# Optimization experiments

Measured on AMD Instinct MI355X. Metric: run time of the kernel, lower is better.

The kernel has to match this reference:

```python
import jax, jax.numpy as jnp
import numpy as np

K = 5
P = 1.5
MU = 0.01
N_NODES = 100000
N_EDGES = 1600000
D_FEAT = 32


def setup_inputs() -> dict:
    key = jax.random.key(0)
    k1, k2 = jax.random.split(key)
    h = jax.random.normal(k1, (N_NODES, D_FEAT), dtype=jnp.float32)
    edge_index = jax.random.randint(k2, (2, N_EDGES), 0, N_NODES, dtype=jnp.int64)
    return {"h": h, "edge_index": edge_index}


def reference(h, edge_index):
    row, col = edge_index[0], edge_index[1]
    for _ in range(K):
        diff = h[row] - h[col]                      # [E, d] gather
        norm_diff = jnp.maximum(jnp.linalg.norm(diff, axis=1), 1e-6)  # [E]
        weights = (norm_diff / norm_diff.max()) ** (P - 2.0)          # [E]
        # agg[r] += sum over edges with row==r of weights * (h[col] - h[row])
        msgs = weights[:, None] * (-diff)           # [E, d]
        agg = jax.ops.segment_sum(msgs, row, num_segments=N_NODES)    # [N, d]
        h = h - MU * agg
    return h
```

## Files before the change

kernel.cpp:

```cpp
#include <hip/hip_runtime.h>

#define NN 100000
#define NE 1600000
#define DF 32
#define KIT 5
#define MU 0.01f
#define NSLOT 256
#define NV4 (NN * DF / 4)
#define ELLW 36
#define AUXCAP 65536
#define NSLICE 8
#define SLICEN (NN / NSLICE)
#define NBLKA (NE / 256)
#define SEGW 64

typedef float f32x4 __attribute__((ext_vector_type(4)));


__global__ __launch_bounds__(256) void zero_kernel(int* __restrict__ p, int n) {
    int i = blockIdx.x * blockDim.x + threadIdx.x;
    if (i < n) p[i] = 0;
}

__global__ __launch_bounds__(256) void ell_part_kernel(const int* __restrict__ row,
                                                       const int* __restrict__ col,
                                                       unsigned int* __restrict__ buck,
                                                       int* __restrict__ cnts,
                                                       int* __restrict__ auxcnt,
                                                       int2* __restrict__ aux) {
    __shared__ int wcnt[4][8];
    __shared__ int woff[4][8];
    const int t = threadIdx.x;
    const int w = t >> 6;
    const int lane = t & 63;
    const int e = blockIdx.x * 256 + t;
    const int r = __builtin_nontemporal_load(&row[e]);
    const int c = __builtin_nontemporal_load(&col[e]);
    const int b = r / SLICEN;
    const int rl = r - b * SLICEN;
    const unsigned int packed = ((unsigned int)rl << 17) | (unsigned int)c;

    int myprefix = 0;
    #pragma unroll
    for (int k = 0; k < 8; ++k) {
        const unsigned long long mk = __ballot(b == k);
        if (lane == 0) wcnt[w][k] = __popcll(mk);
        if (k == b) myprefix = __popcll(mk & ((1ull << lane) - 1ull));
    }
    __syncthreads();
    if (t < 32) {
        const int w2 = t >> 3, k = t & 7;
        int o = 0;
        for (int w3 = 0; w3 < w2; ++w3) o += wcnt[w3][k];
        woff[w2][k] = o;
    }
    if (t < 8) {
        cnts[blockIdx.x * 8 + t] = wcnt[0][t] + wcnt[1][t] + wcnt[2][t] + wcnt[3][t];
    }
    __syncthreads();

    const int pos = woff[w][b] + myprefix;
    if (pos < SEGW) {
        buck[(b * NBLKA + (int)blockIdx.x) * SEGW + pos] = packed;
    } else {
        const int a = atomicAdd(auxcnt, 1);
        if (a < AUXCAP) aux[a] = make_int2(r, c);
    }
}

__global__ __launch_bounds__(256) void ell_fill_kernel(const unsigned int* __restrict__ buck,
                                                       const int* __restrict__ cnts,
                                                       int* __restrict__ degc,
                                                       int* __restrict__ colell,
                                                       int* __restrict__ auxcnt,
                                                       int2* __restrict__ aux) {
    const int s = blockIdx.x & (NSLICE - 1);
    const int g = blockIdx.x >> 3;
    const int ng = gridDim.x >> 3;
    const int t = threadIdx.x;
    const int j = t & 63;
    const int bo = t >> 6;
    const int lo = s * SLICEN;
    for (int blk = g * 4 + bo; blk < NBLKA; blk += ng * 4) {
        const int cnt = min(cnts[blk * 8 + s], SEGW);
        if (j < cnt) {
            const unsigned int pk =
                __builtin_nontemporal_load(&buck[(s * NBLKA + blk) * SEGW + j]);
            const int c = (int)(pk & 0x1ffffu);
            const int r = lo + (int)(pk >> 17);
            const int pos = atomicAdd(&degc[r], 1);
            if (pos < ELLW) {
                colell[r * ELLW + pos] = c;
            } else {
                const int a = atomicAdd(auxcnt, 1);
                if (a < AUXCAP) aux[a] = make_int2(r, c);
            }
        }
    }
}


__device__ __forceinline__ unsigned int pack2bf(float a, float b) {
    unsigned int ua = __float_as_uint(a);
    unsigned int ub = __float_as_uint(b);
    return ((ua + 0x8000u) >> 16) | (((ub + 0x8000u) >> 16) << 16);
}

__device__ __forceinline__ void unpack8(uint4 v, float* f) {
    f[0] = __uint_as_float(v.x << 16);
    f[1] = __uint_as_float(v.x & 0xffff0000u);
    f[2] = __uint_as_float(v.y << 16);
    f[3] = __uint_as_float(v.y & 0xffff0000u);
    f[4] = __uint_as_float(v.z << 16);
    f[5] = __uint_as_float(v.z & 0xffff0000u);
    f[6] = __uint_as_float(v.w << 16);
    f[7] = __uint_as_float(v.w & 0xffff0000u);
}

__device__ __forceinline__ void nt_store4(float* p, float a, float b, float c, float d) {
    f32x4 v = {a, b, c, d};
    __builtin_nontemporal_store(v, (f32x4*)p);
}

__global__ __launch_bounds__(256) void tobf16_kernel(const float* __restrict__ h,
                                                     uint2* __restrict__ hb) {
    int i = blockIdx.x * blockDim.x + threadIdx.x;
    if (i < NV4) {
        const f32x4 v = __builtin_nontemporal_load(((const f32x4*)h) + i);
        hb[i] = make_uint2(pack2bf(v.x, v.y), pack2bf(v.z, v.w));
    }
}


__global__ __launch_bounds__(256) void agg_kernel(const uint4* __restrict__ hb4,
                                                  const int* __restrict__ degc,
                                                  const int* __restrict__ colell,
                                                  float* __restrict__ S,
                                                  int* __restrict__ maxslots) {
    const int lane = threadIdx.x & 31;
    const int q = lane >> 2;
    const int f2 = lane & 3;
    const int pair = (blockIdx.x * blockDim.x + threadIdx.x) >> 5;
    const int n0 = pair * 2;
    const int n1 = n0 + 1;

    const int d0 = min(degc[n0], ELLW);
    const int d1 = min(degc[n1], ELLW);

    const int ca = (lane < d0) ? __builtin_nontemporal_load(&colell[n0 * ELLW + lane]) : n0;
    const int cb = (lane < d1) ? __builtin_nontemporal_load(&colell[n1 * ELLW + lane]) : n1;
    const uint4 hru0 = hb4[n0 * 4 + f2];
    const uint4 hru1 = hb4[n1 * 4 + f2];

    uint4 u0[4], u1[4];
    #pragma unroll
    for (int j = 0; j < 4; ++j) u0[j] = hb4[__shfl(ca, 8 * j + q, 32) * 4 + f2];
    #pragma unroll
    for (int j = 0; j < 4; ++j) u1[j] = hb4[__shfl(cb, 8 * j + q, 32) * 4 + f2];

    float hr0[8], hr1[8];
    unpack8(hru0, hr0);
    unpack8(hru1, hr1);

    float acc0[8], acc1[8];
    #pragma unroll
    for (int i = 0; i < 8; ++i) { acc0[i] = 0.0f; acc1[i] = 0.0f; }
    float nmax = 0.0f;

    #pragma unroll
    for (int j = 0; j < 4; ++j) {
        float d[8];
        unpack8(u0[j], d);
        float s = 0.0f;
        #pragma unroll
        for (int i = 0; i < 8; ++i) {
            d[i] = hr0[i] - d[i];
            s = fmaf(d[i], d[i], s);
        }
        s += __shfl_xor(s, 1, 32);
        s += __shfl_xor(s, 2, 32);
        const float n = fmaxf(sqrtf(s), 1e-6f);
        nmax = fmaxf(nmax, n);
        const float w = rsqrtf(n);
        #pragma unroll
        for (int i = 0; i < 8; ++i) acc0[i] = fmaf(-d[i], w, acc0[i]);
    }
    #pragma unroll
    for (int j = 0; j < 4; ++j) {
        float d[8];
        unpack8(u1[j], d);
        float s = 0.0f;
        #pragma unroll
        for (int i = 0; i < 8; ++i) {
            d[i] = hr1[i] - d[i];
            s = fmaf(d[i], d[i], s);
        }
        s += __shfl_xor(s, 1, 32);
        s += __shfl_xor(s, 2, 32);
        const float n = fmaxf(sqrtf(s), 1e-6f);
        nmax = fmaxf(nmax, n);
        const float w = rsqrtf(n);
        #pragma unroll
        for (int i = 0; i < 8; ++i) acc1[i] = fmaf(-d[i], w, acc1[i]);
    }

    for (int k = 32; k < d0; k += 8) {
        const int ei = k + q;
        const int c = (ei < d0) ? __builtin_nontemporal_load(&colell[n0 * ELLW + ei]) : n0;
        const uint4 uu = hb4[c * 4 + f2];
        float d[8];
        unpack8(uu, d);
        float s = 0.0f;
        #pragma unroll
        for (int i = 0; i < 8; ++i) {
            d[i] = hr0[i] - d[i];
            s = fmaf(d[i], d[i], s);
        }
        s += __shfl_xor(s, 1, 32);
        s += __shfl_xor(s, 2, 32);
        const float n = fmaxf(sqrtf(s), 1e-6f);
        nmax = fmaxf(nmax, n);
        const float w = rsqrtf(n);
        #pragma unroll
        for (int i = 0; i < 8; ++i) acc0[i] = fmaf(-d[i], w, acc0[i]);
    }
    for (int k = 32; k < d1; k += 8) {
        const int ei = k + q;
        const int c = (ei < d1) ? __builtin_nontemporal_load(&colell[n1 * ELLW + ei]) : n1;
        const uint4 uu = hb4[c * 4 + f2];
        float d[8];
        unpack8(uu, d);
        float s = 0.0f;
        #pragma unroll
        for (int i = 0; i < 8; ++i) {
            d[i] = hr1[i] - d[i];
            s = fmaf(d[i], d[i], s);
        }
        s += __shfl_xor(s, 1, 32);
        s += __shfl_xor(s, 2, 32);
        const float n = fmaxf(sqrtf(s), 1e-6f);
        nmax = fmaxf(nmax, n);
        const float w = rsqrtf(n);
        #pragma unroll
        for (int i = 0; i < 8; ++i) acc1[i] = fmaf(-d[i], w, acc1[i]);
    }

    #pragma unroll
    for (int m = 4; m < 32; m <<= 1) {
        #pragma unroll
        for (int i = 0; i < 8; ++i) {
            acc0[i] += __shfl_xor(acc0[i], m, 32);
            acc1[i] += __shfl_xor(acc1[i], m, 32);
        }
    }
    if (q == 0) {
        nt_store4(S + n0 * 32 + f2 * 8,     acc0[0], acc0[1], acc0[2], acc0[3]);
        nt_store4(S + n0 * 32 + f2 * 8 + 4, acc0[4], acc0[5], acc0[6], acc0[7]);
        nt_store4(S + n1 * 32 + f2 * 8,     acc1[0], acc1[1], acc1[2], acc1[3]);
        nt_store4(S + n1 * 32 + f2 * 8 + 4, acc1[4], acc1[5], acc1[6], acc1[7]);
    }

    nmax = fmaxf(nmax, __shfl_xor(nmax, 4, 32));
    nmax = fmaxf(nmax, __shfl_xor(nmax, 8, 32));
    nmax = fmaxf(nmax, __shfl_xor(nmax, 16, 32));
    nmax = fmaxf(nmax, __shfl_xor(nmax, 32, 64));
    if ((threadIdx.x & 63) == 0) {
        atomicMax(&maxslots[blockIdx.x & (NSLOT - 1)], __float_as_int(nmax));
    }
}

__global__ __launch_bounds__(256) void aux_kernel(const uint2* __restrict__ hb,
                                                  const int2* __restrict__ aux,
                                                  const int* __restrict__ auxcnt,
                                                  float* __restrict__ S,
                                                  int* __restrict__ maxslots) {
    const int n = min(*auxcnt, AUXCAP);
    for (int i = blockIdx.x * blockDim.x + threadIdx.x; i < n;
         i += gridDim.x * blockDim.x) {
        const int r = aux[i].x;
        const int c = aux[i].y;
        float d[32];
        float s = 0.0f;
        for (int j = 0; j < 8; ++j) {
            const uint2 ur = hb[r * 8 + j];
            const uint2 uc = hb[c * 8 + j];
            float fr[4], fc[4];
            fr[0] = __uint_as_float(ur.x << 16);
            fr[1] = __uint_as_float(ur.x & 0xffff0000u);
            fr[2] = __uint_as_float(ur.y << 16);
            fr[3] = __uint_as_float(ur.y & 0xffff0000u);
            fc[0] = __uint_as_float(uc.x << 16);
            fc[1] = __uint_as_float(uc.x & 0xffff0000u);
            fc[2] = __uint_as_float(uc.y << 16);
            fc[3] = __uint_as_float(uc.y & 0xffff0000u);
            #pragma unroll
            for (int k = 0; k < 4; ++k) {
                d[j * 4 + k] = fr[k] - fc[k];
                s = fmaf(d[j * 4 + k], d[j * 4 + k], s);
            }
        }
        const float nn = fmaxf(sqrtf(s), 1e-6f);
        atomicMax(&maxslots[i & (NSLOT - 1)], __float_as_int(nn));
        const float w = rsqrtf(nn);
        for (int f = 0; f < 32; ++f) atomicAdd(&S[r * DF + f], -d[f] * w);
    }
}

__global__ __launch_bounds__(256) void update_kernel(const float* __restrict__ hcur,
                                                     float* __restrict__ hnxt,
                                                     uint2* __restrict__ hb,
                                                     const float* __restrict__ S,
                                                     const int* __restrict__ slots) {
    const int t = threadIdx.x;
    int v = slots[t];
    #pragma unroll
    for (int m = 32; m > 0; m >>= 1) v = max(v, __shfl_xor(v, m, 64));
    __shared__ int sm[4];
    __shared__ float sscale;
    if ((t & 63) == 0) sm[t >> 6] = v;
    __syncthreads();
    if (t == 0) {
        int bm = max(max(sm[0], sm[1]), max(sm[2], sm[3]));
        sscale = MU * sqrtf(__int_as_float(bm));
    }
    __syncthreads();
    const float scale = sscale;
    const int i = blockIdx.x * blockDim.x + t;
    if (i < NV4) {
        const f32x4 hv = __builtin_nontemporal_load(((const f32x4*)hcur) + i);
        const f32x4 sv = __builtin_nontemporal_load(((const f32x4*)S) + i);
        const f32x4 o = hv - scale * sv;
        __builtin_nontemporal_store(o, ((f32x4*)hnxt) + i);
        hb[i] = make_uint2(pack2bf(o.x, o.y), pack2bf(o.z, o.w));
    }
}

extern "C" void kernel_launch(void* const* d_in, const int* in_sizes, int n_in,
                              void* d_out, int out_size, void* d_ws, size_t ws_size,
                              hipStream_t stream) {
    const float* h_in = (const float*)d_in[0];
    const int* row = (const int*)d_in[1];
    const int* col = row + NE;
    float* out = (float*)d_out;

    float* S = (float*)d_ws;
    int* maxslots = (int*)(S + NN * DF);
    int* degc = maxslots + KIT * NSLOT;
    int* auxcnt = degc + NN;
    uintptr_t pa = (uintptr_t)(auxcnt + 1);
    pa = (pa + 7) & ~(uintptr_t)7;
    int2* aux = (int2*)pa;
    int* colell = (int*)(aux + AUXCAP);
    uintptr_t p = (uintptr_t)(colell + NN * ELLW);
    p = (p + 15) & ~(uintptr_t)15;
    uint2* hb = (uint2*)p;
    int* cnts = (int*)(hb + NV4);
    unsigned int* buck = (unsigned int*)S;

    const int zb = (NN + 1 + 255) / 256;
    const int fb = NSLICE * 256;
    const int gb = (NN / 2 * 32 + 255) / 256;
    const int ub = (NV4 + 255) / 256;

    zero_kernel<<<zb, 256, 0, stream>>>(degc, NN + 1);
    ell_part_kernel<<<NBLKA, 256, 0, stream>>>(row, col, buck, cnts, auxcnt, aux);
    ell_fill_kernel<<<fb, 256, 0, stream>>>(buck, cnts, degc, colell, auxcnt, aux);
    tobf16_kernel<<<ub, 256, 0, stream>>>(h_in, hb);

    for (int it = 0; it < KIT; ++it) {
        const float* cur = (it == 0) ? h_in : out;
        agg_kernel<<<gb, 256, 0, stream>>>((const uint4*)hb, degc, colell, S,
                                           maxslots + it * NSLOT);
        aux_kernel<<<32, 256, 0, stream>>>(hb, aux, auxcnt, S, maxslots + it * NSLOT);
        update_kernel<<<ub, 256, 0, stream>>>(cur, out, hb, (const float*)S,
                                              maxslots + it * NSLOT);
    }
}
```

Before: 435.1 us.

## Build ELL via per-block LDS staging and shared-memory degree counters per sub-slice

The partition kernel now stages each block's bucketed edges in shared memory, pads them with an invalid marker and writes full 64-entry segments, so the per-block count array is no longer needed. The fill kernel is restructured so each 1024-thread block owns a sub-range of one slice. It scans every segment of that slice, counts degrees with shared-memory atomics and writes degc once at the end, which removes the global degc zeroing and the global atomics. Nontemporal loads and stores in agg and update are replaced with plain vector accesses. The cost is that each fill block reads the whole slice's buckets (20x redundant reads), and cache behaviour changes from dropping the nontemporal hints.

Result: slower. 459.1 us (+5.5%).

```diff
diff --git a/kernel.cpp b/kernel.cpp
--- a/kernel.cpp
+++ b/kernel.cpp
@@ -11,13 +11,16 @@
 #define AUXCAP 65536
 #define NSLICE 8
 #define SLICEN (NN / NSLICE)
+#define NSUB 20
+#define SUBN (SLICEN / NSUB)
 #define NBLKA (NE / 256)
 #define SEGW 64
+#define INVALID_PK 0xffffffffu
 
 typedef float f32x4 __attribute__((ext_vector_type(4)));
 
 
-__global__ __launch_bounds__(256) void zero_kernel(int* __restrict__ p, int n) {
+__global__ __launch_bounds__(64) void zero_kernel(int* __restrict__ p, int n) {
     int i = blockIdx.x * blockDim.x + threadIdx.x;
     if (i < n) p[i] = 0;
 }
@@ -25,14 +28,18 @@
 __global__ __launch_bounds__(256) void ell_part_kernel(const int* __restrict__ row,
                                                        const int* __restrict__ col,
                                                        unsigned int* __restrict__ buck,
-                                                       int* __restrict__ cnts,
                                                        int* __restrict__ auxcnt,
                                                        int2* __restrict__ aux) {
     __shared__ int wcnt[4][8];
     __shared__ int woff[4][8];
+    __shared__ unsigned int sseg[8][SEGW];
     const int t = threadIdx.x;
     const int w = t >> 6;
     const int lane = t & 63;
+
+    ((unsigned int*)sseg)[t] = INVALID_PK;
+    ((unsigned int*)sseg)[t + 256] = INVALID_PK;
+
     const int e = blockIdx.x * 256 + t;
     const int r = __builtin_nontemporal_load(&row[e]);
     const int c = __builtin_nontemporal_load(&col[e]);
@@ -54,41 +61,54 @@
         for (int w3 = 0; w3 < w2; ++w3) o += wcnt[w3][k];
         woff[w2][k] = o;
     }
-    if (t < 8) {
-        cnts[blockIdx.x * 8 + t] = wcnt[0][t] + wcnt[1][t] + wcnt[2][t] + wcnt[3][t];
-    }
     __syncthreads();
 
     const int pos = woff[w][b] + myprefix;
     if (pos < SEGW) {
-        buck[(b * NBLKA + (int)blockIdx.x) * SEGW + pos] = packed;
+        sseg[b][pos] = packed;
     } else {
         const int a = atomicAdd(auxcnt, 1);
         if (a < AUXCAP) aux[a] = make_int2(r, c);
     }
-}
-
-__global__ __launch_bounds__(256) void ell_fill_kernel(const unsigned int* __restrict__ buck,
-                                                       const int* __restrict__ cnts,
-                                                       int* __restrict__ degc,
-                                                       int* __restrict__ colell,
-                                                       int* __restrict__ auxcnt,
-                                                       int2* __restrict__ aux) {
+    __syncthreads();
+
+    #pragma unroll
+    for (int k = 0; k < 2; ++k) {
+        const int idx = t + k * 256;
+        const int bb = idx >> 6;
+        const int j = idx & 63;
+        buck[((size_t)bb * NBLKA + blockIdx.x) * SEGW + j] = sseg[bb][j];
+    }
+}
+
+__global__ __launch_bounds__(1024) void ell_fill_kernel(const unsigned int* __restrict__ buck,
+                                                        int* __restrict__ degc,
+                                                        int* __restrict__ colell,
+                                                        int* __restrict__ auxcnt,
+                                                        int2* __restrict__ aux) {
+    __shared__ int lcnt[SUBN];
+    const int t = threadIdx.x;
     const int s = blockIdx.x & (NSLICE - 1);
-    const int g = blockIdx.x >> 3;
-    const int ng = gridDim.x >> 3;
-    const int t = threadIdx.x;
-    const int j = t & 63;
-    const int bo = t >> 6;
-    const int lo = s * SLICEN;
-    for (int blk = g * 4 + bo; blk < NBLKA; blk += ng * 4) {
-        const int cnt = min(cnts[blk * 8 + s], SEGW);
-        if (j < cnt) {
-            const unsigned int pk =
-                __builtin_nontemporal_load(&buck[(s * NBLKA + blk) * SEGW + j]);
+    const int sub = blockIdx.x >> 3;
+    const int lane = t & 63;
+    const int wid = t >> 6;
+    const int lo = sub * SUBN;
+    const int hi = lo + SUBN;
+
+    for (int i = t; i < SUBN; i += 1024) lcnt[i] = 0;
+    __syncthreads();
+
+    const unsigned int* sp = buck + (size_t)s * NBLKA * SEGW;
+    int blk = wid;
+    unsigned int pk = sp[(size_t)blk * SEGW + lane];
+    for (; blk < NBLKA; blk += 16) {
+        const int nb = blk + 16;
+        const unsigned int nx = (nb < NBLKA) ? sp[(size_t)nb * SEGW + lane] : INVALID_PK;
+        const int rl = (int)(pk >> 17);
+        if (rl >= lo && rl < hi) {
             const int c = (int)(pk & 0x1ffffu);
-            const int r = lo + (int)(pk >> 17);
-            const int pos = atomicAdd(&degc[r], 1);
+            const int pos = atomicAdd(&lcnt[rl - lo], 1);
+            const int r = s * SLICEN + rl;
             if (pos < ELLW) {
                 colell[r * ELLW + pos] = c;
             } else {
@@ -96,7 +116,10 @@
                 if (a < AUXCAP) aux[a] = make_int2(r, c);
             }
         }
-    }
+        pk = nx;
+    }
+    __syncthreads();
+    for (int i = t; i < SUBN; i += 1024) degc[s * SLICEN + lo + i] = lcnt[i];
 }
 
 
@@ -115,11 +138,6 @@
     f[5] = __uint_as_float(v.z & 0xffff0000u);
     f[6] = __uint_as_float(v.w << 16);
     f[7] = __uint_as_float(v.w & 0xffff0000u);
-}
-
-__device__ __forceinline__ void nt_store4(float* p, float a, float b, float c, float d) {
-    f32x4 v = {a, b, c, d};
-    __builtin_nontemporal_store(v, (f32x4*)p);
 }
 
 __global__ __launch_bounds__(256) void tobf16_kernel(const float* __restrict__ h,
@@ -254,10 +272,10 @@
         }
     }
     if (q == 0) {
-        nt_store4(S + n0 * 32 + f2 * 8,     acc0[0], acc0[1], acc0[2], acc0[3]);
-        nt_store4(S + n0 * 32 + f2 * 8 + 4, acc0[4], acc0[5], acc0[6], acc0[7]);
-        nt_store4(S + n1 * 32 + f2 * 8,     acc1[0], acc1[1], acc1[2], acc1[3]);
-        nt_store4(S + n1 * 32 + f2 * 8 + 4, acc1[4], acc1[5], acc1[6], acc1[7]);
+        ((float4*)S)[n0 * 8 + f2 * 2] = make_float4(acc0[0], acc0[1], acc0[2], acc0[3]);
+        ((float4*)S)[n0 * 8 + f2 * 2 + 1] = make_float4(acc0[4], acc0[5], acc0[6], acc0[7]);
+        ((float4*)S)[n1 * 8 + f2 * 2] = make_float4(acc1[0], acc1[1], acc1[2], acc1[3]);
+        ((float4*)S)[n1 * 8 + f2 * 2 + 1] = make_float4(acc1[4], acc1[5], acc1[6], acc1[7]);
     }
 
     nmax = fmaxf(nmax, __shfl_xor(nmax, 4, 32));
@@ -306,10 +324,10 @@
     }
 }
 
-__global__ __launch_bounds__(256) void update_kernel(const float* __restrict__ hcur,
-                                                     float* __restrict__ hnxt,
+__global__ __launch_bounds__(256) void update_kernel(const float4* __restrict__ hcur,
+                                                     float4* __restrict__ hnxt,
                                                      uint2* __restrict__ hb,
-                                                     const float* __restrict__ S,
+                                                     const float4* __restrict__ S,
                                                      const int* __restrict__ slots) {
     const int t = threadIdx.x;
     int v = slots[t];
@@ -327,10 +345,14 @@
     const float scale = sscale;
     const int i = blockIdx.x * blockDim.x + t;
     if (i < NV4) {
-        const f32x4 hv = __builtin_nontemporal_load(((const f32x4*)hcur) + i);
-        const f32x4 sv = __builtin_nontemporal_load(((const f32x4*)S) + i);
-        const f32x4 o = hv - scale * sv;
-        __builtin_nontemporal_store(o, ((f32x4*)hnxt) + i);
+        const float4 hv = hcur[i];
+        const float4 sv = S[i];
+        float4 o;
+        o.x = hv.x - scale * sv.x;
+        o.y = hv.y - scale * sv.y;
+        o.z = hv.z - scale * sv.z;
+        o.w = hv.w - scale * sv.w;
+        hnxt[i] = o;
         hb[i] = make_uint2(pack2bf(o.x, o.y), pack2bf(o.z, o.w));
     }
 }
@@ -354,17 +376,15 @@
     uintptr_t p = (uintptr_t)(colell + NN * ELLW);
     p = (p + 15) & ~(uintptr_t)15;
     uint2* hb = (uint2*)p;
-    int* cnts = (int*)(hb + NV4);
     unsigned int* buck = (unsigned int*)S;
 
-    const int zb = (NN + 1 + 255) / 256;
-    const int fb = NSLICE * 256;
+    const int fb = NSLICE * NSUB;
     const int gb = (NN / 2 * 32 + 255) / 256;
     const int ub = (NV4 + 255) / 256;
 
-    zero_kernel<<<zb, 256, 0, stream>>>(degc, NN + 1);
-    ell_part_kernel<<<NBLKA, 256, 0, stream>>>(row, col, buck, cnts, auxcnt, aux);
-    ell_fill_kernel<<<fb, 256, 0, stream>>>(buck, cnts, degc, colell, auxcnt, aux);
+    zero_kernel<<<1, 64, 0, stream>>>(auxcnt, 1);
+    ell_part_kernel<<<NBLKA, 256, 0, stream>>>(row, col, buck, auxcnt, aux);
+    ell_fill_kernel<<<fb, 1024, 0, stream>>>(buck, degc, colell, auxcnt, aux);
     tobf16_kernel<<<ub, 256, 0, stream>>>(h_in, hb);
 
     for (int it = 0; it < KIT; ++it) {
@@ -372,7 +392,8 @@
         agg_kernel<<<gb, 256, 0, stream>>>((const uint4*)hb, degc, colell, S,
                                            maxslots + it * NSLOT);
         aux_kernel<<<32, 256, 0, stream>>>(hb, aux, auxcnt, S, maxslots + it * NSLOT);
-        update_kernel<<<ub, 256, 0, stream>>>(cur, out, hb, (const float*)S,
+        update_kernel<<<ub, 256, 0, stream>>>((const float4*)cur, (float4*)out, hb,
+                                              (const float4*)S,
                                               maxslots + it * NSLOT);
     }
 }
```
